# Optimization experiments

Measured on AMD Instinct MI355X. Metric: run time of the kernel, lower is better.

Reference implementation:

```python
import jax, jax.numpy as jnp
import numpy as np

NUM_LAYERS = 2
INPUT_SIZE = 256
HIDDEN_SIZE = 512
OUTPUT_SIZE = 256
BATCH = 32
SEQ = 2048


def setup_inputs() -> dict:
    key = jax.random.key(0)
    ks = jax.random.split(key, 12)
    s = 1.0 / np.sqrt(HIDDEN_SIZE)
    H4 = 4 * HIDDEN_SIZE
    x = jax.random.normal(ks[0], (BATCH, SEQ, INPUT_SIZE), dtype=jnp.float32)
    # layer 0: input_size -> hidden; layer 1: hidden -> hidden (torch gate order i,f,g,o)
    w_ih0 = jax.random.uniform(ks[1], (H4, INPUT_SIZE), minval=-s, maxval=s)
    w_hh0 = jax.random.uniform(ks[2], (H4, HIDDEN_SIZE), minval=-s, maxval=s)
    b0 = jax.random.uniform(ks[3], (H4,), minval=-s, maxval=s)  # b_ih0 + b_hh0 combined
    w_ih1 = jax.random.uniform(ks[4], (H4, HIDDEN_SIZE), minval=-s, maxval=s)
    w_hh1 = jax.random.uniform(ks[5], (H4, HIDDEN_SIZE), minval=-s, maxval=s)
    b1 = jax.random.uniform(ks[6], (H4,), minval=-s, maxval=s)
    w_fc = jax.random.uniform(ks[7], (OUTPUT_SIZE, HIDDEN_SIZE), minval=-s, maxval=s)
    b_fc = jax.random.uniform(ks[8], (OUTPUT_SIZE,), minval=-s, maxval=s)
    return {"x": x, "w_ih0": w_ih0, "w_hh0": w_hh0, "b0": b0,
            "w_ih1": w_ih1, "w_hh1": w_hh1, "b1": b1,
            "w_fc": w_fc, "b_fc": b_fc}


def _lstm_layer(x, w_ih, w_hh, b):
    # x: [B, T, In] -> output hidden sequence [B, T, H]
    B = x.shape[0]
    H = w_hh.shape[1]
    # precompute all input projections: [T, B, 4H]
    xg = (jnp.einsum('bti,gi->btg', x, w_ih) + b).transpose(1, 0, 2)

    def step(carry, xg_t):
        h, c = carry
        gates = xg_t + h @ w_hh.T  # [B, 4H]
        i, f, g, o = jnp.split(gates, 4, axis=-1)
        i = jax.nn.sigmoid(i)
        f = jax.nn.sigmoid(f)
        g = jnp.tanh(g)
        o = jax.nn.sigmoid(o)
        c = f * c + i * g
        h = o * jnp.tanh(c)
        return (h, c), h

    h0 = jnp.zeros((B, H), dtype=x.dtype)
    c0 = jnp.zeros((B, H), dtype=x.dtype)
    _, hs = jax.lax.scan(step, (h0, c0), xg)  # hs: [T, B, H]
    return hs.transpose(1, 0, 2)


def reference(x, w_ih0, w_hh0, b0, w_ih1, w_hh1, b1, w_fc, b_fc):
    h = _lstm_layer(x, w_ih0, w_hh0, b0)
    h = _lstm_layer(h, w_ih1, w_hh1, b1)
    return jnp.einsum('bth,oh->bto', h, w_fc) + b_fc
```

## Files before the change

### kernel.cpp

```cpp
#include <hip/hip_runtime.h>

typedef __attribute__((ext_vector_type(8))) short bf16x8;
typedef __attribute__((ext_vector_type(4))) float f32x4;
typedef __attribute__((ext_vector_type(4))) unsigned int u32x4;

#define T_SEQ 2048
#define RING  64
#define NL0   32
#define NL1   32
#define NFC   8
#define NWG   (NL0 + NL1 + NFC)
#define SLOT_STRIDE 16
#define NEG_INF (-1000000)

#define HSWZ(o) ((o) ^ ((((o) >> 10) & 7) << 4))

static __device__ __forceinline__ unsigned short f2b(float f) {
  unsigned u = __float_as_uint(f);
  u = (u + 0x7fffu + ((u >> 16) & 1u)) >> 16;
  return (unsigned short)u;
}
static __device__ __forceinline__ float sigm(float x) { return 1.f / (1.f + __expf(-x)); }
static __device__ __forceinline__ float tanh_f(float x) { return 2.f / (1.f + __expf(-2.f * x)) - 1.f; }

static __device__ __forceinline__ u32x4 llc_load16(const void* p) {
  u32x4 v;
  asm volatile("global_load_dwordx4 %0, %1, off sc0 sc1" : "=v"(v) : "v"(p) : "memory");
  return v;
}
static __device__ __forceinline__ void llc_store4(void* p, unsigned v) {
  asm volatile("global_store_dword %0, %1, off sc0 sc1" :: "v"(p), "v"(v) : "memory");
}
static __device__ __forceinline__ void vmwait() {
  asm volatile("s_waitcnt vmcnt(0)" ::: "memory");
}
static __device__ __forceinline__ int flag_ld(const int* p) {
  return __hip_atomic_load(p, __ATOMIC_RELAXED, __HIP_MEMORY_SCOPE_SYSTEM);
}
static __device__ __forceinline__ void flag_st(int* p, int v) {
  __hip_atomic_store(p, v, __ATOMIC_RELAXED, __HIP_MEMORY_SCOPE_SYSTEM);
}

static __device__ void spin_flags(const int* s0, int n0, const int* s1, int n1,
                                  const int* sf, int nf) {
  if (threadIdx.x < 64) {
    const int lane = threadIdx.x;
    const int* p1 = (lane < 32) ? (s0 + lane * SLOT_STRIDE) : (s1 + (lane - 32) * SLOT_STRIDE);
    const int need1 = (lane < 32) ? n0 : n1;
    const int* p2 = sf + (lane & 7) * SLOT_STRIDE;
    const bool chk2 = (lane < 8) && (nf > NEG_INF);
    for (;;) {
      int v1 = flag_ld(p1);
      int v2 = chk2 ? flag_ld(p2) : 0x7fffffff;
      int ok = (v1 >= need1) && (!chk2 || (v2 >= nf));
      if (__all(ok)) break;
    }
  }
  __syncthreads();
}

__global__ void lstm_prologue(
    const float* __restrict__ x, const float* __restrict__ wih0, const float* __restrict__ whh0,
    const float* __restrict__ wih1, const float* __restrict__ whh1, const float* __restrict__ wfc,
    unsigned short* __restrict__ wl0, unsigned short* __restrict__ wl1,
    unsigned short* __restrict__ wfcp, unsigned short* __restrict__ xb,
    unsigned short* __restrict__ h0r, unsigned short* __restrict__ h1r,
    int* __restrict__ flags) {
  size_t tid = (size_t)blockIdx.x * blockDim.x + threadIdx.x;
  size_t nthr = (size_t)gridDim.x * blockDim.x;
  for (size_t i = tid; i < (size_t)2048 * 768; i += nthr) {
    int r = (int)(i / 768), k = (int)(i % 768);
    float v = (k < 256) ? wih0[(size_t)r * 256 + k] : whh0[(size_t)r * 512 + (k - 256)];
    wl0[i] = f2b(v);
  }
  for (size_t i = tid; i < (size_t)2048 * 1024; i += nthr) {
    int r = (int)(i >> 10), k = (int)(i & 1023);
    float v = (k < 512) ? wih1[((size_t)r << 9) + k] : whh1[((size_t)r << 9) + (k - 512)];
    wl1[i] = f2b(v);
  }
  for (size_t i = tid; i < 131072; i += nthr) wfcp[i] = f2b(wfc[i]);
  for (size_t i = tid; i < (size_t)16777216; i += nthr) {
    int ii = (int)(i & 255), b = (int)((i >> 8) & 31), t = (int)(i >> 13);
    xb[i] = f2b(x[((size_t)b * 2048 + t) * 256 + ii]);
  }
  for (size_t i = tid; i < (size_t)NWG * SLOT_STRIDE; i += nthr) flags[i] = 0;
  for (size_t i = tid; i < 32 * 512; i += nthr) {
    h0r[(size_t)(RING - 1) * 32 * 512 + i] = 0;
    h1r[(size_t)(RING - 1) * 32 * 512 + i] = 0;
  }
}

template <int ISL0>
static __device__ void lstm_path(
    const unsigned short* __restrict__ xb, const unsigned short* __restrict__ wl,
    const float* __restrict__ bias,
    unsigned short* __restrict__ h0r, unsigned short* __restrict__ h1r,
    int* s0, int* s1, int* sf, int wid2,
    unsigned short* hA, unsigned short* xA, float (*gates)[32][18]) {
  const int tid = threadIdx.x;
  const int wave = tid >> 6, lane = tid & 63, l15 = lane & 15, kgrp = lane >> 4;
  const int u0 = wid2 * 16;
  constexpr int K = ISL0 ? 768 : 1024;
  constexpr int NKW = ISL0 ? 24 : 32;
  const unsigned short* wrow = wl + (size_t)(wave * 512 + u0 + l15) * K;

  bf16x8 wf[NKW];
#pragma unroll
  for (int kk = 0; kk < NKW; ++kk) wf[kk] = *(const bf16x8*)(wrow + kk * 32 + kgrp * 8);

  const int ue = 2 * (tid & 7);
  const int be = tid >> 3;
  const float bi0 = bias[0 * 512 + u0 + ue], bi1 = bias[0 * 512 + u0 + ue + 1];
  const float bf0 = bias[1 * 512 + u0 + ue], bf1 = bias[1 * 512 + u0 + ue + 1];
  const float bg0 = bias[2 * 512 + u0 + ue], bg1 = bias[2 * 512 + u0 + ue + 1];
  const float bo0 = bias[3 * 512 + u0 + ue], bo1 = bias[3 * 512 + u0 + ue + 1];
  float cc0 = 0.f, cc1 = 0.f;
  unsigned short* myring = ISL0 ? h0r : h1r;
  int* myslot = (ISL0 ? s0 : s1) + wid2 * SLOT_STRIDE;

  for (int t = 0; t < T_SEQ; ++t) {
    f32x4 acc0 = {0.f, 0.f, 0.f, 0.f}, acc1 = {0.f, 0.f, 0.f, 0.f};

    if (ISL0) {
      bf16x8 xf0[8], xf1[8];
      const unsigned short* xt = xb + (size_t)t * (32 * 256);
#pragma unroll
      for (int kk = 0; kk < 8; ++kk) {
        xf0[kk] = *(const bf16x8*)(xt + l15 * 256 + kk * 32 + kgrp * 8);
        xf1[kk] = *(const bf16x8*)(xt + (16 + l15) * 256 + kk * 32 + kgrp * 8);
      }
      spin_flags(s0, t, s1, t - (RING - 1), sf, NEG_INF);

      const unsigned short* hprev = myring + (size_t)((t - 1) & (RING - 1)) * (32 * 512);
      u32x4 th[8];
#pragma unroll
      for (int k = 0; k < 8; ++k)
        th[k] = llc_load16((const char*)hprev + (size_t)(tid + k * 256) * 16);
#pragma unroll
      for (int kk = 0; kk < 8; ++kk) {
        acc0 = __builtin_amdgcn_mfma_f32_16x16x32_bf16(xf0[kk], wf[kk], acc0, 0, 0, 0);
        acc1 = __builtin_amdgcn_mfma_f32_16x16x32_bf16(xf1[kk], wf[kk], acc1, 0, 0, 0);
      }
      vmwait();
#pragma unroll
      for (int k = 0; k < 8; ++k) {
        int off = (tid + k * 256) * 16;
        *(u32x4*)((char*)hA + HSWZ(off)) = th[k];
      }
      __syncthreads();
#pragma unroll
      for (int kk = 0; kk < 16; ++kk) {
        int cb = (kk * 32 + kgrp * 8) * 2;
        bf16x8 a0 = *(const bf16x8*)((const char*)hA + HSWZ(l15 * 1024 + cb));
        bf16x8 a1 = *(const bf16x8*)((const char*)hA + HSWZ((16 + l15) * 1024 + cb));
        acc0 = __builtin_amdgcn_mfma_f32_16x16x32_bf16(a0, wf[8 + kk], acc0, 0, 0, 0);
        acc1 = __builtin_amdgcn_mfma_f32_16x16x32_bf16(a1, wf[8 + kk], acc1, 0, 0, 0);
      }
    } else {
      spin_flags(s0, t + 1, s1, NEG_INF, sf, NEG_INF);
      const unsigned short* h0cur = h0r + (size_t)(t & (RING - 1)) * (32 * 512);
      u32x4 tx[8];
#pragma unroll
      for (int k = 0; k < 8; ++k)
        tx[k] = llc_load16((const char*)h0cur + (size_t)(tid + k * 256) * 16);
      vmwait();
#pragma unroll
      for (int k = 0; k < 8; ++k) {
        int off = (tid + k * 256) * 16;
        *(u32x4*)((char*)xA + HSWZ(off)) = tx[k];
      }
      __syncthreads();
#pragma unroll
      for (int kk = 0; kk < 16; ++kk) {
        int cb = (kk * 32 + kgrp * 8) * 2;
        bf16x8 a0 = *(const bf16x8*)((const char*)xA + HSWZ(l15 * 1024 + cb));
        bf16x8 a1 = *(const bf16x8*)((const char*)xA + HSWZ((16 + l15) * 1024 + cb));
        acc0 = __builtin_amdgcn_mfma_f32_16x16x32_bf16(a0, wf[kk], acc0, 0, 0, 0);
        acc1 = __builtin_amdgcn_mfma_f32_16x16x32_bf16(a1, wf[kk], acc1, 0, 0, 0);
      }

      spin_flags(s0, NEG_INF, s1, t, sf, t - (RING - 1));
      const unsigned short* hprev = myring + (size_t)((t - 1) & (RING - 1)) * (32 * 512);
      u32x4 th[8];
#pragma unroll
      for (int k = 0; k < 8; ++k)
        th[k] = llc_load16((const char*)hprev + (size_t)(tid + k * 256) * 16);
      vmwait();
#pragma unroll
      for (int k = 0; k < 8; ++k) {
        int off = (tid + k * 256) * 16;
        *(u32x4*)((char*)hA + HSWZ(off)) = th[k];
      }
      __syncthreads();
#pragma unroll
      for (int kk = 0; kk < 16; ++kk) {
        int cb = (kk * 32 + kgrp * 8) * 2;
        bf16x8 a0 = *(const bf16x8*)((const char*)hA + HSWZ(l15 * 1024 + cb));
        bf16x8 a1 = *(const bf16x8*)((const char*)hA + HSWZ((16 + l15) * 1024 + cb));
        acc0 = __builtin_amdgcn_mfma_f32_16x16x32_bf16(a0, wf[16 + kk], acc0, 0, 0, 0);
        acc1 = __builtin_amdgcn_mfma_f32_16x16x32_bf16(a1, wf[16 + kk], acc1, 0, 0, 0);
      }
    }

#pragma unroll
    for (int j = 0; j < 4; ++j) {
      gates[wave][kgrp * 4 + j][l15] = acc0[j];
      gates[wave][16 + kgrp * 4 + j][l15] = acc1[j];
    }
    __syncthreads();

    unsigned short* hdst = myring + (size_t)(t & (RING - 1)) * (32 * 512);
    float i0 = sigm(gates[0][be][ue] + bi0);
    float ff0 = sigm(gates[1][be][ue] + bf0);
    float g0 = tanh_f(gates[2][be][ue] + bg0);
    float o0 = sigm(gates[3][be][ue] + bo0);
    cc0 = ff0 * cc0 + i0 * g0;
    float hv0 = o0 * tanh_f(cc0);
    float i1 = sigm(gates[0][be][ue + 1] + bi1);
    float ff1 = sigm(gates[1][be][ue + 1] + bf1);
    float g1 = tanh_f(gates[2][be][ue + 1] + bg1);
    float o1 = sigm(gates[3][be][ue + 1] + bo1);
    cc1 = ff1 * cc1 + i1 * g1;
    float hv1 = o1 * tanh_f(cc1);
    unsigned pv = (unsigned)f2b(hv0) | ((unsigned)f2b(hv1) << 16);
    llc_store4(hdst + (size_t)be * 512 + u0 + ue, pv);
    vmwait();
    __syncthreads();
    if (tid == 0) flag_st(myslot, t + 1);
  }
}

__global__ void __launch_bounds__(256) lstm_main(
    const unsigned short* __restrict__ xb,
    const unsigned short* __restrict__ wl0,
    const unsigned short* __restrict__ wl1,
    const unsigned short* __restrict__ wfcp,
    const float* __restrict__ b0,
    const float* __restrict__ b1,
    const float* __restrict__ bfc,
    unsigned short* __restrict__ h0r,
    unsigned short* __restrict__ h1r,
    int* flags,
    float* __restrict__ out) {
  __shared__ __align__(16) unsigned short hA[32 * 512];
  __shared__ __align__(16) unsigned short xA[32 * 512];
  __shared__ __align__(16) float gates[4][32][18];
  const int tid = threadIdx.x;
  const int wave = tid >> 6, lane = tid & 63, l15 = lane & 15, kgrp = lane >> 4;
  const int wid = blockIdx.x;
  int* s0 = flags;
  int* s1 = flags + NL0 * SLOT_STRIDE;
  int* sf = flags + (NL0 + NL1) * SLOT_STRIDE;

  if (wid < NL0) {
    lstm_path<1>(xb, wl0, b0, h0r, h1r, s0, s1, sf, wid, hA, xA, gates);
  } else if (wid < NL0 + NL1) {
    lstm_path<0>(xb, wl1, b1, h0r, h1r, s0, s1, sf, wid - NL0, hA, xA, gates);
  } else {
    const int fcw = wid - NL0 - NL1;
    const int mt = wave >> 1, ntile = wave & 1;
    const int orow = fcw * 32 + ntile * 16 + l15;
    bf16x8 wff[16];
#pragma unroll
    for (int kk = 0; kk < 16; ++kk)
      wff[kk] = *(const bf16x8*)(wfcp + (size_t)orow * 512 + kk * 32 + kgrp * 8);
    const float bb = bfc[orow];
    for (int t = 0; t < T_SEQ; ++t) {
      spin_flags(s0, NEG_INF, s1, t + 1, sf, NEG_INF);
      const unsigned short* hcur = h1r + (size_t)(t & (RING - 1)) * (32 * 512);
      u32x4 th[8];
#pragma unroll
      for (int k = 0; k < 8; ++k)
        th[k] = llc_load16((const char*)hcur + (size_t)(tid + k * 256) * 16);
      vmwait();
#pragma unroll
      for (int k = 0; k < 8; ++k) {
        int off = (tid + k * 256) * 16;
        *(u32x4*)((char*)hA + HSWZ(off)) = th[k];
      }
      __syncthreads();
      if (tid == 0) flag_st(sf + fcw * SLOT_STRIDE, t + 1);
      f32x4 acc = {0.f, 0.f, 0.f, 0.f};
#pragma unroll
      for (int kk = 0; kk < 16; ++kk) {
        int row = mt * 16 + l15;
        bf16x8 a = *(const bf16x8*)((const char*)hA + HSWZ(row * 1024 + (kk * 32 + kgrp * 8) * 2));
        acc = __builtin_amdgcn_mfma_f32_16x16x32_bf16(a, wff[kk], acc, 0, 0, 0);
      }
#pragma unroll
      for (int j = 0; j < 4; ++j) {
        int b = mt * 16 + kgrp * 4 + j;
        out[((size_t)b * T_SEQ + t) * 256 + orow] = acc[j] + bb;
      }
    }
  }
}

extern "C" void kernel_launch(void* const* d_in, const int* in_sizes, int n_in,
                              void* d_out, int out_size, void* d_ws, size_t ws_size,
                              hipStream_t stream) {
  const float* x    = (const float*)d_in[0];
  const float* wih0 = (const float*)d_in[1];
  const float* whh0 = (const float*)d_in[2];
  const float* b0   = (const float*)d_in[3];
  const float* wih1 = (const float*)d_in[4];
  const float* whh1 = (const float*)d_in[5];
  const float* b1   = (const float*)d_in[6];
  const float* wfc  = (const float*)d_in[7];
  const float* bfc  = (const float*)d_in[8];
  float* outp = (float*)d_out;

  char* ws = (char*)d_ws;
  size_t off = 0;
  unsigned short* wl0p = (unsigned short*)(ws + off); off += (size_t)2048 * 768 * 2;
  unsigned short* wl1p = (unsigned short*)(ws + off); off += (size_t)2048 * 1024 * 2;
  unsigned short* wfcp = (unsigned short*)(ws + off); off += (size_t)256 * 512 * 2;
  unsigned short* xbp  = (unsigned short*)(ws + off); off += (size_t)2048 * 32 * 256 * 2;
  unsigned short* h0rp = (unsigned short*)(ws + off); off += (size_t)RING * 32 * 512 * 2;
  unsigned short* h1rp = (unsigned short*)(ws + off); off += (size_t)RING * 32 * 512 * 2;
  int* flagsp = (int*)(ws + off); off += (size_t)NWG * SLOT_STRIDE * sizeof(int);

  lstm_prologue<<<dim3(1024), dim3(256), 0, stream>>>(
      x, wih0, whh0, wih1, whh1, wfc, wl0p, wl1p, wfcp, xbp, h0rp, h1rp, flagsp);

  lstm_main<<<dim3(NWG), dim3(256), 0, stream>>>(
      xbp, wl0p, wl1p, wfcp, b0, b1, bfc, h0rp, h1rp, flagsp, outp);
}
```

Before: 8.478 ms.

## Halve workgroup count with 512-thread blocks owning 32 hidden units each

Workgroups now run 512 threads (8 waves) and each LSTM workgroup owns 32 hidden units instead of 16, so each layer uses 16 workgroups and the FC stage uses 4. This halves the number of flags every step must poll and the number of workgroups that reload each h slice from the LLC, cutting the per-timestep cross-workgroup sync cost. The gate scratch buffer grows to 8 tiles, and the FC path alternates between two LDS buffers. In exchange each workgroup holds twice the weight fragments per CU, which raises register pressure and may add per-step latency.

```diff
diff --git a/kernel.cpp b/kernel.cpp
--- a/kernel.cpp
+++ b/kernel.cpp
@@ -6,10 +6,9 @@
 
 #define T_SEQ 2048
 #define RING  64
-#define NL0   32
-#define NL1   32
-#define NFC   8
-#define NWG   (NL0 + NL1 + NFC)
+#define LWG   16
+#define FWG   4
+#define NWG   (LWG + LWG + FWG)
 #define SLOT_STRIDE 16
 #define NEG_INF (-1000000)
 
@@ -45,14 +44,17 @@
                                   const int* sf, int nf) {
   if (threadIdx.x < 64) {
     const int lane = threadIdx.x;
-    const int* p1 = (lane < 32) ? (s0 + lane * SLOT_STRIDE) : (s1 + (lane - 32) * SLOT_STRIDE);
-    const int need1 = (lane < 32) ? n0 : n1;
-    const int* p2 = sf + (lane & 7) * SLOT_STRIDE;
-    const bool chk2 = (lane < 8) && (nf > NEG_INF);
+    const bool g1 = (lane < 16) && (n0 > NEG_INF);
+    const bool g2 = (lane >= 32) && (lane < 48) && (n1 > NEG_INF);
+    const int* p1 = g1 ? (s0 + lane * SLOT_STRIDE)
+                       : (g2 ? (s1 + (lane - 32) * SLOT_STRIDE) : s0);
+    const int need1 = g1 ? n0 : n1;
+    const int* p2 = sf + (lane & 3) * SLOT_STRIDE;
+    const bool chk2 = (lane < 4) && (nf > NEG_INF);
     for (;;) {
-      int v1 = flag_ld(p1);
+      int v1 = (g1 || g2) ? flag_ld(p1) : 0x7fffffff;
       int v2 = chk2 ? flag_ld(p2) : 0x7fffffff;
-      int ok = (v1 >= need1) && (!chk2 || (v2 >= nf));
+      int ok = (!(g1 || g2) || (v1 >= need1)) && (!chk2 || (v2 >= nf));
       if (__all(ok)) break;
     }
   }
@@ -99,17 +101,21 @@
     unsigned short* hA, unsigned short* xA, float (*gates)[32][18]) {
   const int tid = threadIdx.x;
   const int wave = tid >> 6, lane = tid & 63, l15 = lane & 15, kgrp = lane >> 4;
-  const int u0 = wid2 * 16;
+  const int u0 = wid2 * 32;
   constexpr int K = ISL0 ? 768 : 1024;
   constexpr int NKW = ISL0 ? 24 : 32;
-  const unsigned short* wrow = wl + (size_t)(wave * 512 + u0 + l15) * K;
+  const int grow = (wave & 3) * 512 + u0 + ((wave >> 2) << 4);
+  const unsigned short* wrow = wl + (size_t)(grow + l15) * K;
 
   bf16x8 wf[NKW];
 #pragma unroll
-  for (int kk = 0; kk < NKW; ++kk) wf[kk] = *(const bf16x8*)(wrow + kk * 32 + kgrp * 8);
-
-  const int ue = 2 * (tid & 7);
-  const int be = tid >> 3;
+  for (int kk = 0; kk < NKW; ++kk) {
+    wf[kk] = *(const bf16x8*)(wrow + kk * 32 + kgrp * 8);
+    asm volatile("" : "+v"(wf[kk]));
+  }
+
+  const int ue = 2 * (tid & 15);
+  const int be = tid >> 4;
   const float bi0 = bias[0 * 512 + u0 + ue], bi1 = bias[0 * 512 + u0 + ue + 1];
   const float bf0 = bias[1 * 512 + u0 + ue], bf1 = bias[1 * 512 + u0 + ue + 1];
   const float bg0 = bias[2 * 512 + u0 + ue], bg1 = bias[2 * 512 + u0 + ue + 1];
@@ -132,10 +138,10 @@
       spin_flags(s0, t, s1, t - (RING - 1), sf, NEG_INF);
 
       const unsigned short* hprev = myring + (size_t)((t - 1) & (RING - 1)) * (32 * 512);
-      u32x4 th[8];
-#pragma unroll
-      for (int k = 0; k < 8; ++k)
-        th[k] = llc_load16((const char*)hprev + (size_t)(tid + k * 256) * 16);
+      u32x4 th[4];
+#pragma unroll
+      for (int k = 0; k < 4; ++k)
+        th[k] = llc_load16((const char*)hprev + (size_t)(tid + k * 512) * 16);
 #pragma unroll
       for (int kk = 0; kk < 8; ++kk) {
         acc0 = __builtin_amdgcn_mfma_f32_16x16x32_bf16(xf0[kk], wf[kk], acc0, 0, 0, 0);
@@ -143,8 +149,8 @@
       }
       vmwait();
 #pragma unroll
-      for (int k = 0; k < 8; ++k) {
-        int off = (tid + k * 256) * 16;
+      for (int k = 0; k < 4; ++k) {
+        int off = (tid + k * 512) * 16;
         *(u32x4*)((char*)hA + HSWZ(off)) = th[k];
       }
       __syncthreads();
@@ -159,14 +165,14 @@
     } else {
       spin_flags(s0, t + 1, s1, NEG_INF, sf, NEG_INF);
       const unsigned short* h0cur = h0r + (size_t)(t & (RING - 1)) * (32 * 512);
-      u32x4 tx[8];
-#pragma unroll
-      for (int k = 0; k < 8; ++k)
-        tx[k] = llc_load16((const char*)h0cur + (size_t)(tid + k * 256) * 16);
+      u32x4 tx[4];
+#pragma unroll
+      for (int k = 0; k < 4; ++k)
+        tx[k] = llc_load16((const char*)h0cur + (size_t)(tid + k * 512) * 16);
       vmwait();
 #pragma unroll
-      for (int k = 0; k < 8; ++k) {
-        int off = (tid + k * 256) * 16;
+      for (int k = 0; k < 4; ++k) {
+        int off = (tid + k * 512) * 16;
         *(u32x4*)((char*)xA + HSWZ(off)) = tx[k];
       }
       __syncthreads();
@@ -181,14 +187,14 @@
 
       spin_flags(s0, NEG_INF, s1, t, sf, t - (RING - 1));
       const unsigned short* hprev = myring + (size_t)((t - 1) & (RING - 1)) * (32 * 512);
-      u32x4 th[8];
-#pragma unroll
-      for (int k = 0; k < 8; ++k)
-        th[k] = llc_load16((const char*)hprev + (size_t)(tid + k * 256) * 16);
+      u32x4 th[4];
+#pragma unroll
+      for (int k = 0; k < 4; ++k)
+        th[k] = llc_load16((const char*)hprev + (size_t)(tid + k * 512) * 16);
       vmwait();
 #pragma unroll
-      for (int k = 0; k < 8; ++k) {
-        int off = (tid + k * 256) * 16;
+      for (int k = 0; k < 4; ++k) {
+        int off = (tid + k * 512) * 16;
         *(u32x4*)((char*)hA + HSWZ(off)) = th[k];
       }
       __syncthreads();
@@ -210,16 +216,18 @@
     __syncthreads();
 
     unsigned short* hdst = myring + (size_t)(t & (RING - 1)) * (32 * 512);
-    float i0 = sigm(gates[0][be][ue] + bi0);
-    float ff0 = sigm(gates[1][be][ue] + bf0);
-    float g0 = tanh_f(gates[2][be][ue] + bg0);
-    float o0 = sigm(gates[3][be][ue] + bo0);
+    const int wb = (ue >> 4) << 2;
+    const int ul = ue & 15;
+    float i0 = sigm(gates[0 + wb][be][ul] + bi0);
+    float ff0 = sigm(gates[1 + wb][be][ul] + bf0);
+    float g0 = tanh_f(gates[2 + wb][be][ul] + bg0);
+    float o0 = sigm(gates[3 + wb][be][ul] + bo0);
     cc0 = ff0 * cc0 + i0 * g0;
     float hv0 = o0 * tanh_f(cc0);
-    float i1 = sigm(gates[0][be][ue + 1] + bi1);
-    float ff1 = sigm(gates[1][be][ue + 1] + bf1);
-    float g1 = tanh_f(gates[2][be][ue + 1] + bg1);
-    float o1 = sigm(gates[3][be][ue + 1] + bo1);
+    float i1 = sigm(gates[0 + wb][be][ul + 1] + bi1);
+    float ff1 = sigm(gates[1 + wb][be][ul + 1] + bf1);
+    float g1 = tanh_f(gates[2 + wb][be][ul + 1] + bg1);
+    float o1 = sigm(gates[3 + wb][be][ul + 1] + bo1);
     cc1 = ff1 * cc1 + i1 * g1;
     float hv1 = o1 * tanh_f(cc1);
     unsigned pv = (unsigned)f2b(hv0) | ((unsigned)f2b(hv1) << 16);
@@ -230,7 +238,7 @@
   }
 }
 
-__global__ void __launch_bounds__(256) lstm_main(
+__global__ void __launch_bounds__(512, 1) lstm_main(
     const unsigned short* __restrict__ xb,
     const unsigned short* __restrict__ wl0,
     const unsigned short* __restrict__ wl1,
@@ -244,39 +252,42 @@
     float* __restrict__ out) {
   __shared__ __align__(16) unsigned short hA[32 * 512];
   __shared__ __align__(16) unsigned short xA[32 * 512];
-  __shared__ __align__(16) float gates[4][32][18];
+  __shared__ __align__(16) float gates[8][32][18];
   const int tid = threadIdx.x;
   const int wave = tid >> 6, lane = tid & 63, l15 = lane & 15, kgrp = lane >> 4;
   const int wid = blockIdx.x;
   int* s0 = flags;
-  int* s1 = flags + NL0 * SLOT_STRIDE;
-  int* sf = flags + (NL0 + NL1) * SLOT_STRIDE;
-
-  if (wid < NL0) {
+  int* s1 = flags + LWG * SLOT_STRIDE;
+  int* sf = flags + 2 * LWG * SLOT_STRIDE;
+
+  if (wid < LWG) {
     lstm_path<1>(xb, wl0, b0, h0r, h1r, s0, s1, sf, wid, hA, xA, gates);
-  } else if (wid < NL0 + NL1) {
-    lstm_path<0>(xb, wl1, b1, h0r, h1r, s0, s1, sf, wid - NL0, hA, xA, gates);
+  } else if (wid < 2 * LWG) {
+    lstm_path<0>(xb, wl1, b1, h0r, h1r, s0, s1, sf, wid - LWG, hA, xA, gates);
   } else {
-    const int fcw = wid - NL0 - NL1;
-    const int mt = wave >> 1, ntile = wave & 1;
-    const int orow = fcw * 32 + ntile * 16 + l15;
+    const int fcw = wid - 2 * LWG;
+    const int mt = wave >> 2, rtile = wave & 3;
+    const int orow = fcw * 64 + rtile * 16 + l15;
     bf16x8 wff[16];
 #pragma unroll
-    for (int kk = 0; kk < 16; ++kk)
+    for (int kk = 0; kk < 16; ++kk) {
       wff[kk] = *(const bf16x8*)(wfcp + (size_t)orow * 512 + kk * 32 + kgrp * 8);
+      asm volatile("" : "+v"(wff[kk]));
+    }
     const float bb = bfc[orow];
     for (int t = 0; t < T_SEQ; ++t) {
       spin_flags(s0, NEG_INF, s1, t + 1, sf, NEG_INF);
       const unsigned short* hcur = h1r + (size_t)(t & (RING - 1)) * (32 * 512);
-      u32x4 th[8];
-#pragma unroll
-      for (int k = 0; k < 8; ++k)
-        th[k] = llc_load16((const char*)hcur + (size_t)(tid + k * 256) * 16);
+      unsigned short* buf = (t & 1) ? xA : hA;
+      u32x4 th[4];
+#pragma unroll
+      for (int k = 0; k < 4; ++k)
+        th[k] = llc_load16((const char*)hcur + (size_t)(tid + k * 512) * 16);
       vmwait();
 #pragma unroll
-      for (int k = 0; k < 8; ++k) {
-        int off = (tid + k * 256) * 16;
-        *(u32x4*)((char*)hA + HSWZ(off)) = th[k];
+      for (int k = 0; k < 4; ++k) {
+        int off = (tid + k * 512) * 16;
+        *(u32x4*)((char*)buf + HSWZ(off)) = th[k];
       }
       __syncthreads();
       if (tid == 0) flag_st(sf + fcw * SLOT_STRIDE, t + 1);
@@ -284,7 +295,7 @@
 #pragma unroll
       for (int kk = 0; kk < 16; ++kk) {
         int row = mt * 16 + l15;
-        bf16x8 a = *(const bf16x8*)((const char*)hA + HSWZ(row * 1024 + (kk * 32 + kgrp * 8) * 2));
+        bf16x8 a = *(const bf16x8*)((const char*)buf + HSWZ(row * 1024 + (kk * 32 + kgrp * 8) * 2));
         acc = __builtin_amdgcn_mfma_f32_16x16x32_bf16(a, wff[kk], acc, 0, 0, 0);
       }
 #pragma unroll
@@ -323,6 +334,6 @@
   lstm_prologue<<<dim3(1024), dim3(256), 0, stream>>>(
       x, wih0, whh0, wih1, whh1, wfc, wl0p, wl1p, wfcp, xbp, h0rp, h1rp, flagsp);
 
-  lstm_main<<<dim3(NWG), dim3(256), 0, stream>>>(
+  lstm_main<<<dim3(NWG), dim3(512), 0, stream>>>(
       xbp, wl0p, wl1p, wfcp, b0, b1, bfc, h0rp, h1rp, flagsp, outp);
 }
```

After: 12.98 ms. 53.1% more time.

## Move recurrent weights into LDS and stream layer-1 input weights from global

Applied to the files above, without the earlier changes.

The per-wave register-resident weight fragments (up to 32 bf16x8 per lane) are replaced. The recurrent W_hh slice now sits in a 64KB shared-memory buffer and is read per k-step. Layer 1's input-projection weights are instead reloaded from global/L2 every timestep. The goal is to relieve register pressure and spilling. The cost is extra LDS and global traffic on the serial recurrence critical path, plus much higher LDS usage per block. The FC blocks also double-buffer their staging buffer across timesteps, which removes a write-after-read hazard.

```diff
diff --git a/kernel.cpp b/kernel.cpp
--- a/kernel.cpp
+++ b/kernel.cpp
@@ -96,17 +96,36 @@
     const float* __restrict__ bias,
     unsigned short* __restrict__ h0r, unsigned short* __restrict__ h1r,
     int* s0, int* s1, int* sf, int wid2,
-    unsigned short* hA, unsigned short* xA, float (*gates)[32][18]) {
+    unsigned short* hA, unsigned short* xA, unsigned short* wB,
+    float (*gates)[32][18]) {
   const int tid = threadIdx.x;
   const int wave = tid >> 6, lane = tid & 63, l15 = lane & 15, kgrp = lane >> 4;
   const int u0 = wid2 * 16;
   constexpr int K = ISL0 ? 768 : 1024;
-  constexpr int NKW = ISL0 ? 24 : 32;
-  const unsigned short* wrow = wl + (size_t)(wave * 512 + u0 + l15) * K;
-
-  bf16x8 wf[NKW];
-#pragma unroll
-  for (int kk = 0; kk < NKW; ++kk) wf[kk] = *(const bf16x8*)(wrow + kk * 32 + kgrp * 8);
+  constexpr int KOFF = ISL0 ? 256 : 512;
+
+  for (int c = tid; c < 4096; c += 256) {
+    int off = c * 16;
+    int r = off >> 10;
+    int kb = off & 1023;
+    int grow = (r >> 4) * 512 + u0 + (r & 15);
+    u32x4 v = *(const u32x4*)(wl + (size_t)grow * K + KOFF + (kb >> 1));
+    *(u32x4*)((char*)wB + HSWZ(off)) = v;
+  }
+
+  bf16x8 wfx[8];
+  if (ISL0) {
+    const unsigned short* wrow = wl + (size_t)(wave * 512 + u0 + l15) * K;
+#pragma unroll
+    for (int kk = 0; kk < 8; ++kk) {
+      wfx[kk] = *(const bf16x8*)(wrow + kk * 32 + kgrp * 8);
+      asm volatile("" : "+v"(wfx[kk]));
+    }
+  }
+  __syncthreads();
+
+  const int wrow_lds = (wave * 16 + l15) * 1024;
+  const unsigned short* wrow0 = wl + (size_t)(wave * 512 + u0 + l15) * K;
 
   const int ue = 2 * (tid & 7);
   const int be = tid >> 3;
@@ -138,8 +157,8 @@
         th[k] = llc_load16((const char*)hprev + (size_t)(tid + k * 256) * 16);
 #pragma unroll
       for (int kk = 0; kk < 8; ++kk) {
-        acc0 = __builtin_amdgcn_mfma_f32_16x16x32_bf16(xf0[kk], wf[kk], acc0, 0, 0, 0);
-        acc1 = __builtin_amdgcn_mfma_f32_16x16x32_bf16(xf1[kk], wf[kk], acc1, 0, 0, 0);
+        acc0 = __builtin_amdgcn_mfma_f32_16x16x32_bf16(xf0[kk], wfx[kk], acc0, 0, 0, 0);
+        acc1 = __builtin_amdgcn_mfma_f32_16x16x32_bf16(xf1[kk], wfx[kk], acc1, 0, 0, 0);
       }
       vmwait();
 #pragma unroll
@@ -151,10 +170,11 @@
 #pragma unroll
       for (int kk = 0; kk < 16; ++kk) {
         int cb = (kk * 32 + kgrp * 8) * 2;
+        bf16x8 bw = *(const bf16x8*)((const char*)wB + HSWZ(wrow_lds + cb));
         bf16x8 a0 = *(const bf16x8*)((const char*)hA + HSWZ(l15 * 1024 + cb));
         bf16x8 a1 = *(const bf16x8*)((const char*)hA + HSWZ((16 + l15) * 1024 + cb));
-        acc0 = __builtin_amdgcn_mfma_f32_16x16x32_bf16(a0, wf[8 + kk], acc0, 0, 0, 0);
-        acc1 = __builtin_amdgcn_mfma_f32_16x16x32_bf16(a1, wf[8 + kk], acc1, 0, 0, 0);
+        acc0 = __builtin_amdgcn_mfma_f32_16x16x32_bf16(a0, bw, acc0, 0, 0, 0);
+        acc1 = __builtin_amdgcn_mfma_f32_16x16x32_bf16(a1, bw, acc1, 0, 0, 0);
       }
     } else {
       spin_flags(s0, t + 1, s1, NEG_INF, sf, NEG_INF);
@@ -172,11 +192,12 @@
       __syncthreads();
 #pragma unroll
       for (int kk = 0; kk < 16; ++kk) {
+        bf16x8 bw = *(const bf16x8*)(wrow0 + kk * 32 + kgrp * 8);
         int cb = (kk * 32 + kgrp * 8) * 2;
         bf16x8 a0 = *(const bf16x8*)((const char*)xA + HSWZ(l15 * 1024 + cb));
         bf16x8 a1 = *(const bf16x8*)((const char*)xA + HSWZ((16 + l15) * 1024 + cb));
-        acc0 = __builtin_amdgcn_mfma_f32_16x16x32_bf16(a0, wf[kk], acc0, 0, 0, 0);
-        acc1 = __builtin_amdgcn_mfma_f32_16x16x32_bf16(a1, wf[kk], acc1, 0, 0, 0);
+        acc0 = __builtin_amdgcn_mfma_f32_16x16x32_bf16(a0, bw, acc0, 0, 0, 0);
+        acc1 = __builtin_amdgcn_mfma_f32_16x16x32_bf16(a1, bw, acc1, 0, 0, 0);
       }
 
       spin_flags(s0, NEG_INF, s1, t, sf, t - (RING - 1));
@@ -195,10 +216,11 @@
 #pragma unroll
       for (int kk = 0; kk < 16; ++kk) {
         int cb = (kk * 32 + kgrp * 8) * 2;
+        bf16x8 bw = *(const bf16x8*)((const char*)wB + HSWZ(wrow_lds + cb));
         bf16x8 a0 = *(const bf16x8*)((const char*)hA + HSWZ(l15 * 1024 + cb));
         bf16x8 a1 = *(const bf16x8*)((const char*)hA + HSWZ((16 + l15) * 1024 + cb));
-        acc0 = __builtin_amdgcn_mfma_f32_16x16x32_bf16(a0, wf[16 + kk], acc0, 0, 0, 0);
-        acc1 = __builtin_amdgcn_mfma_f32_16x16x32_bf16(a1, wf[16 + kk], acc1, 0, 0, 0);
+        acc0 = __builtin_amdgcn_mfma_f32_16x16x32_bf16(a0, bw, acc0, 0, 0, 0);
+        acc1 = __builtin_amdgcn_mfma_f32_16x16x32_bf16(a1, bw, acc1, 0, 0, 0);
       }
     }
 
@@ -244,6 +266,7 @@
     float* __restrict__ out) {
   __shared__ __align__(16) unsigned short hA[32 * 512];
   __shared__ __align__(16) unsigned short xA[32 * 512];
+  __shared__ __align__(16) unsigned short wB[64 * 512];
   __shared__ __align__(16) float gates[4][32][18];
   const int tid = threadIdx.x;
   const int wave = tid >> 6, lane = tid & 63, l15 = lane & 15, kgrp = lane >> 4;
@@ -253,9 +276,9 @@
   int* sf = flags + (NL0 + NL1) * SLOT_STRIDE;
 
   if (wid < NL0) {
-    lstm_path<1>(xb, wl0, b0, h0r, h1r, s0, s1, sf, wid, hA, xA, gates);
+    lstm_path<1>(xb, wl0, b0, h0r, h1r, s0, s1, sf, wid, hA, xA, wB, gates);
   } else if (wid < NL0 + NL1) {
-    lstm_path<0>(xb, wl1, b1, h0r, h1r, s0, s1, sf, wid - NL0, hA, xA, gates);
+    lstm_path<0>(xb, wl1, b1, h0r, h1r, s0, s1, sf, wid - NL0, hA, xA, wB, gates);
   } else {
     const int fcw = wid - NL0 - NL1;
     const int mt = wave >> 1, ntile = wave & 1;
@@ -268,6 +291,7 @@
     for (int t = 0; t < T_SEQ; ++t) {
       spin_flags(s0, NEG_INF, s1, t + 1, sf, NEG_INF);
       const unsigned short* hcur = h1r + (size_t)(t & (RING - 1)) * (32 * 512);
+      unsigned short* buf = (t & 1) ? xA : hA;
       u32x4 th[8];
 #pragma unroll
       for (int k = 0; k < 8; ++k)
@@ -276,7 +300,7 @@
 #pragma unroll
       for (int k = 0; k < 8; ++k) {
         int off = (tid + k * 256) * 16;
-        *(u32x4*)((char*)hA + HSWZ(off)) = th[k];
+        *(u32x4*)((char*)buf + HSWZ(off)) = th[k];
       }
       __syncthreads();
       if (tid == 0) flag_st(sf + fcw * SLOT_STRIDE, t + 1);
@@ -284,7 +308,7 @@
 #pragma unroll
       for (int kk = 0; kk < 16; ++kk) {
         int row = mt * 16 + l15;
-        bf16x8 a = *(const bf16x8*)((const char*)hA + HSWZ(row * 1024 + (kk * 32 + kgrp * 8) * 2));
+        bf16x8 a = *(const bf16x8*)((const char*)buf + HSWZ(row * 1024 + (kk * 32 + kgrp * 8) * 2));
         acc = __builtin_amdgcn_mfma_f32_16x16x32_bf16(a, wff[kk], acc, 0, 0, 0);
       }
 #pragma unroll
```

Result: slower. 11.12 ms (+31.1%).
